# Kernel tuning notes

Hardware: AMD Instinct MI355X
Metric: run time of the kernel (lower is better)

## Reference

```python
import jax, jax.numpy as jnp
import numpy as np

B, N, C, E, K = 2, 1024, 128, 64, 20

def setup_inputs() -> dict:
    key = jax.random.key(0)
    ks = jax.random.split(key, 4)
    x = jax.random.normal(ks[0], (B, N, C), dtype=jnp.float32)
    Wl = jax.random.normal(ks[1], (C, E), dtype=jnp.float32) * 0.05
    Wr = jax.random.normal(ks[2], (C, E), dtype=jnp.float32) * 0.05
    att = jax.random.normal(ks[3], (1, E), dtype=jnp.float32) * 0.1
    bl = jnp.zeros((E,), dtype=jnp.float32)
    br = jnp.zeros((E,), dtype=jnp.float32)
    edge_index = jnp.zeros((2, 1), dtype=jnp.int64)
    batch = jnp.zeros((B * N,), dtype=jnp.int64)
    return {"x": x, "Wl": Wl, "bl": bl, "Wr": Wr, "br": br, "att": att,
            "edge_index": edge_index, "batch": batch}

def reference(x, Wl, bl, Wr, br, att, edge_index, batch):
    # x: [B, N, C]
    b, n, _ = x.shape
    x_l = x @ Wl + bl              # [B, N, E]
    x_r = x @ Wr + br              # [B, N, E]
    # dense pairwise scores: leaky_relu(x_l_i + x_r_j) . att  -> [B, N, N]
    x_cat = jax.nn.leaky_relu(x_l[:, :, None, :] + x_r[:, None, :, :], 0.2)
    alpha = jnp.einsum('bijd,d->bij', x_cat, att[0])
    alpha = jnp.nan_to_num(alpha, nan=0.0, posinf=0.0, neginf=0.0)
    k = min(K, n)
    vals, idx = jax.lax.top_k(alpha, k)            # [B, N, k]
    attention = jax.nn.softmax(vals, axis=-1).reshape(-1)  # [B*N*k]
    # edge index construction (dropout p used only in training; eval = identity)
    offset = (jnp.arange(b) * n)[:, None]                      # [B, 1]
    index_i = jnp.tile(jnp.repeat(jnp.arange(n), k)[None, :], (b, 1)) + offset
    index_j = idx.reshape(b, n * k) + offset
    new_edge_index = jnp.stack([index_i.reshape(-1), index_j.reshape(-1)], axis=0)
    return new_edge_index, attention
```

## Files before the change

### kernel.cpp

```cpp
#include <hip/hip_runtime.h>

#define Bq 2
#define Nq 1024
#define Cq 128
#define Eq 64
#define Kq 20
#define TI 8
#define THREADS 512

__global__ __launch_bounds__(128) void proj_kernel(
    const float* __restrict__ x, const float* __restrict__ Wl,
    const float* __restrict__ bl, const float* __restrict__ Wr,
    const float* __restrict__ br, const float* __restrict__ att,
    float* __restrict__ xl, float* __restrict__ xrT, float* __restrict__ rdot) {
  const int row = blockIdx.x;
  const int t = threadIdx.x;
  __shared__ float xs[Cq];
  xs[t] = x[(size_t)row * Cq + t];
  __syncthreads();
  const float* W = (t < Eq) ? Wl : Wr;
  const int e = t & 63;
  float acc = 0.f;
#pragma unroll 8
  for (int c = 0; c < Cq; ++c) acc += xs[c] * W[c * Eq + e];
  acc += (t < Eq) ? bl[e] : br[e];
  if (t < Eq) {
    xl[(size_t)row * Eq + e] = acc;
  } else {
    xrT[(size_t)e * (Bq * Nq) + row] = acc;
    float rd = acc * att[e];
#pragma unroll
    for (int m = 1; m < 64; m <<= 1) rd += __shfl_xor(rd, m);
    if (e == 0) rdot[row] = rd;
  }
}

__global__ __launch_bounds__(THREADS) void attn_kernel(
    const float* __restrict__ xl, const float* __restrict__ xrT,
    const float* __restrict__ rdot, const float* __restrict__ att,
    float* __restrict__ out) {
  const int gi0  = blockIdx.x * TI;
  const int b    = gi0 >> 10;
  const int tid  = threadIdx.x;
  const int lane = tid & 63;
  const int wave = tid >> 6;

  __shared__ float alpha[TI][Nq];
  __shared__ float xls[TI][Eq];
  __shared__ float catt[Eq];

  xls[tid >> 6][tid & 63] = xl[(size_t)gi0 * Eq + tid];
  if (tid < Eq) catt[tid] = 0.4f * att[tid];
  __syncthreads();

  {
    const int j = tid * 2;
    const float2 rd = *(const float2*)&rdot[b * Nq + j];
    float acc[TI][2];
#pragma unroll
    for (int r = 0; r < TI; ++r) { acc[r][0] = 0.6f * rd.x; acc[r][1] = 0.6f * rd.y; }
    const float* __restrict__ xrb = xrT + (size_t)b * Nq + j;
#pragma unroll
    for (int ch = 0; ch < 16; ++ch) {
      const float4 cv = *(const float4*)&catt[ch * 4];
      float4 xlv[TI];
#pragma unroll
      for (int r = 0; r < TI; ++r) xlv[r] = *(const float4*)&xls[r][ch * 4];
#pragma unroll
      for (int dd = 0; dd < 4; ++dd) {
        const float2 xv = *(const float2*)&xrb[(size_t)(ch * 4 + dd) * (Bq * Nq)];
        const float c = ((const float*)&cv)[dd];
#pragma unroll
        for (int r = 0; r < TI; ++r) {
          const float xld = ((const float*)&xlv[r])[dd];
          acc[r][0] = fmaf(fabsf(xld + xv.x), c, acc[r][0]);
          acc[r][1] = fmaf(fabsf(xld + xv.y), c, acc[r][1]);
        }
      }
    }
#pragma unroll
    for (int r = 0; r < TI; ++r)
      *(float2*)&alpha[r][j] = make_float2(acc[r][0], acc[r][1]);
  }
  __syncthreads();

  const int r = wave;
  float vals[16];
#pragma unroll
  for (int s = 0; s < 16; ++s) vals[s] = alpha[r][lane + 64 * s];
  float lv = -3.4e38f; int li = 0;
#pragma unroll
  for (int s = 0; s < 16; ++s) if (vals[s] > lv) { lv = vals[s]; li = s; }

  float m0 = 0.f, ssum = 0.f, myv = 0.f;
  int myi = 0;
  for (int round = 0; round < Kq; ++round) {
    float bv = lv;
    int   bi = (li << 6) | lane;
#pragma unroll
    for (int mm = 1; mm < 64; mm <<= 1) {
      const float ov = __shfl_xor(bv, mm);
      const int   oi = __shfl_xor(bi, mm);
      if (ov > bv || (ov == bv && oi < bi)) { bv = ov; bi = oi; }
    }
    if (round == 0) m0 = bv;
    ssum += __expf(bv - m0);
    if (lane == round) { myv = bv; myi = bi; }
    if ((bi & 63) == lane) {
#pragma unroll
      for (int s = 0; s < 16; ++s) vals[s] = (s == li) ? -3.4e38f : vals[s];
      lv = -3.4e38f; li = 0;
#pragma unroll
      for (int s = 0; s < 16; ++s) if (vals[s] > lv) { lv = vals[s]; li = s; }
    }
  }

  if (lane < Kq) {
    const int gi = gi0 + r;
    const float p = __expf(myv - m0) / ssum;
    const int base = gi * Kq + lane;
    out[base]                    = (float)gi;
    out[Bq * Nq * Kq + base]     = (float)(b * Nq + myi);
    out[2 * Bq * Nq * Kq + base] = p;
  }
}

extern "C" void kernel_launch(void* const* d_in, const int* in_sizes, int n_in,
                              void* d_out, int out_size, void* d_ws, size_t ws_size,
                              hipStream_t stream) {
  const float* x   = (const float*)d_in[0];
  const float* Wl  = (const float*)d_in[1];
  const float* bl  = (const float*)d_in[2];
  const float* Wr  = (const float*)d_in[3];
  const float* br  = (const float*)d_in[4];
  const float* att = (const float*)d_in[5];
  float* out = (float*)d_out;

  float* xl   = (float*)d_ws;
  float* xrT  = xl + (size_t)Bq * Nq * Eq;
  float* rdot = xrT + (size_t)Eq * Bq * Nq;

  proj_kernel<<<Bq * Nq, Cq, 0, stream>>>(x, Wl, bl, Wr, br, att, xl, xrT, rdot);
  attn_kernel<<<(Bq * Nq) / TI, THREADS, 0, stream>>>(xl, xrT, rdot, att, out);
}
```

Baseline: 42.53 us.

## Retile projection and score kernels, use DPP reductions for top-k selection

The projection kernel now computes four rows per block, reading x directly as float4 instead of staging it in shared memory, and reduces rdot with DPP and readlane instead of shuffles. The score kernel uses a 4x4 register tile per thread with float4 loads of xrT and rescales scores by 1/0.4, folding the 0.4 factor into the softmax exponent. The top-k argmax replaces the 6-step shuffle butterfly with DPP max and min-key reductions. This cuts shuffle latency and per-row launch overhead, but the fewer projection blocks lower parallelism and the scaling trick changes rounding slightly.

Result: faster. 41.29 us (-2.9%).

```diff
diff --git a/kernel.cpp b/kernel.cpp
--- a/kernel.cpp
+++ b/kernel.cpp
@@ -6,36 +6,75 @@
 #define Eq 64
 #define Kq 20
 #define TI 8
-#define THREADS 512
+#define BNK (Bq * Nq * Kq)
+#define NEGF (-3.0e38f)
+
+#define DPP_F(x, ctrl) __int_as_float(__builtin_amdgcn_update_dpp( \
+    __float_as_int(x), __float_as_int(x), (ctrl), 0xf, 0xf, false))
+#define DPP_I(x, ctrl) __builtin_amdgcn_update_dpp((x), (x), (ctrl), 0xf, 0xf, false)
+#define RL_F(x, l) __int_as_float(__builtin_amdgcn_readlane(__float_as_int(x), (l)))
+#define RL_I(x, l) __builtin_amdgcn_readlane((x), (l))
+#define QP_XOR1 0xB1
+#define QP_XOR2 0x4E
+#define ROR4    0x124
+#define ROR8    0x128
 
 __global__ __launch_bounds__(128) void proj_kernel(
     const float* __restrict__ x, const float* __restrict__ Wl,
     const float* __restrict__ bl, const float* __restrict__ Wr,
     const float* __restrict__ br, const float* __restrict__ att,
     float* __restrict__ xl, float* __restrict__ xrT, float* __restrict__ rdot) {
-  const int row = blockIdx.x;
+  const int r0 = blockIdx.x * 4;
   const int t = threadIdx.x;
-  __shared__ float xs[Cq];
-  xs[t] = x[(size_t)row * Cq + t];
-  __syncthreads();
-  const float* W = (t < Eq) ? Wl : Wr;
   const int e = t & 63;
-  float acc = 0.f;
+  const bool left = (t < 64);
+  const float* __restrict__ W = left ? Wl : Wr;
+  const float* __restrict__ xrow = x + (size_t)r0 * Cq;
+
+  float acc[4] = {0.f, 0.f, 0.f, 0.f};
 #pragma unroll 8
-  for (int c = 0; c < Cq; ++c) acc += xs[c] * W[c * Eq + e];
-  acc += (t < Eq) ? bl[e] : br[e];
-  if (t < Eq) {
-    xl[(size_t)row * Eq + e] = acc;
+  for (int c4 = 0; c4 < Cq / 4; ++c4) {
+    const float4 xa = *(const float4*)&xrow[c4 * 4];
+    const float4 xb = *(const float4*)&xrow[Cq + c4 * 4];
+    const float4 xc = *(const float4*)&xrow[2 * Cq + c4 * 4];
+    const float4 xd = *(const float4*)&xrow[3 * Cq + c4 * 4];
+    const float a0[4] = {xa.x, xa.y, xa.z, xa.w};
+    const float a1[4] = {xb.x, xb.y, xb.z, xb.w};
+    const float a2[4] = {xc.x, xc.y, xc.z, xc.w};
+    const float a3[4] = {xd.x, xd.y, xd.z, xd.w};
+#pragma unroll
+    for (int dd = 0; dd < 4; ++dd) {
+      const float w = W[(c4 * 4 + dd) * Eq + e];
+      acc[0] = fmaf(a0[dd], w, acc[0]);
+      acc[1] = fmaf(a1[dd], w, acc[1]);
+      acc[2] = fmaf(a2[dd], w, acc[2]);
+      acc[3] = fmaf(a3[dd], w, acc[3]);
+    }
+  }
+  const float bias = left ? bl[e] : br[e];
+#pragma unroll
+  for (int k = 0; k < 4; ++k) acc[k] += bias;
+
+  if (left) {
+#pragma unroll
+    for (int k = 0; k < 4; ++k) xl[(size_t)(r0 + k) * Eq + e] = acc[k];
   } else {
-    xrT[(size_t)e * (Bq * Nq) + row] = acc;
-    float rd = acc * att[e];
-#pragma unroll
-    for (int m = 1; m < 64; m <<= 1) rd += __shfl_xor(rd, m);
-    if (e == 0) rdot[row] = rd;
+    const float ae = att[e];
+#pragma unroll
+    for (int k = 0; k < 4; ++k) {
+      xrT[(size_t)e * (Bq * Nq) + r0 + k] = acc[k];
+      float s = acc[k] * ae;
+      s += DPP_F(s, QP_XOR1);
+      s += DPP_F(s, QP_XOR2);
+      s += DPP_F(s, ROR4);
+      s += DPP_F(s, ROR8);
+      const float sd = (RL_F(s, 0) + RL_F(s, 16)) + (RL_F(s, 32) + RL_F(s, 48));
+      if (e == 0) rdot[r0 + k] = sd;
+    }
   }
 }
 
-__global__ __launch_bounds__(THREADS) void attn_kernel(
+__global__ __launch_bounds__(512) void attn_kernel(
     const float* __restrict__ xl, const float* __restrict__ xrT,
     const float* __restrict__ rdot, const float* __restrict__ att,
     float* __restrict__ out) {
@@ -47,81 +86,103 @@
 
   __shared__ float alpha[TI][Nq];
   __shared__ float xls[TI][Eq];
-  __shared__ float catt[Eq];
 
   xls[tid >> 6][tid & 63] = xl[(size_t)gi0 * Eq + tid];
-  if (tid < Eq) catt[tid] = 0.4f * att[tid];
   __syncthreads();
 
   {
-    const int j = tid * 2;
-    const float2 rd = *(const float2*)&rdot[b * Nq + j];
-    float acc[TI][2];
-#pragma unroll
-    for (int r = 0; r < TI; ++r) { acc[r][0] = 0.6f * rd.x; acc[r][1] = 0.6f * rd.y; }
-    const float* __restrict__ xrb = xrT + (size_t)b * Nq + j;
-#pragma unroll
+    const int jt = tid & 255;
+    const int j0 = jt * 4;
+    const int rg = tid >> 8;
+    const float4 rd4 = *(const float4*)&rdot[b * Nq + j0];
+    const float rdv[4] = {rd4.x, rd4.y, rd4.z, rd4.w};
+    float acc[4][4];
+#pragma unroll
+    for (int rr = 0; rr < 4; ++rr)
+#pragma unroll
+      for (int jj = 0; jj < 4; ++jj) acc[rr][jj] = 1.5f * rdv[jj];
+
+    const float* __restrict__ xrb = xrT + (size_t)b * Nq + j0;
     for (int ch = 0; ch < 16; ++ch) {
-      const float4 cv = *(const float4*)&catt[ch * 4];
-      float4 xlv[TI];
-#pragma unroll
-      for (int r = 0; r < TI; ++r) xlv[r] = *(const float4*)&xls[r][ch * 4];
+      const float4 av4 = *(const float4*)&att[ch * 4];
+      const float av[4] = {av4.x, av4.y, av4.z, av4.w};
+      float xlr[4][4];
+#pragma unroll
+      for (int rr = 0; rr < 4; ++rr) {
+        const float4 v = *(const float4*)&xls[rg * 4 + rr][ch * 4];
+        xlr[rr][0] = v.x; xlr[rr][1] = v.y; xlr[rr][2] = v.z; xlr[rr][3] = v.w;
+      }
 #pragma unroll
       for (int dd = 0; dd < 4; ++dd) {
-        const float2 xv = *(const float2*)&xrb[(size_t)(ch * 4 + dd) * (Bq * Nq)];
-        const float c = ((const float*)&cv)[dd];
-#pragma unroll
-        for (int r = 0; r < TI; ++r) {
-          const float xld = ((const float*)&xlv[r])[dd];
-          acc[r][0] = fmaf(fabsf(xld + xv.x), c, acc[r][0]);
-          acc[r][1] = fmaf(fabsf(xld + xv.y), c, acc[r][1]);
+        const float4 xv4 = *(const float4*)&xrb[(size_t)(ch * 4 + dd) * (Bq * Nq)];
+        const float xv[4] = {xv4.x, xv4.y, xv4.z, xv4.w};
+        const float a = av[dd];
+#pragma unroll
+        for (int rr = 0; rr < 4; ++rr) {
+          const float xld = xlr[rr][dd];
+#pragma unroll
+          for (int jj = 0; jj < 4; ++jj)
+            acc[rr][jj] = fmaf(fabsf(xld + xv[jj]), a, acc[rr][jj]);
         }
       }
     }
 #pragma unroll
-    for (int r = 0; r < TI; ++r)
-      *(float2*)&alpha[r][j] = make_float2(acc[r][0], acc[r][1]);
+    for (int rr = 0; rr < 4; ++rr)
+      *(float4*)&alpha[rg * 4 + rr][j0] =
+          make_float4(acc[rr][0], acc[rr][1], acc[rr][2], acc[rr][3]);
   }
   __syncthreads();
 
-  const int r = wave;
   float vals[16];
 #pragma unroll
-  for (int s = 0; s < 16; ++s) vals[s] = alpha[r][lane + 64 * s];
-  float lv = -3.4e38f; int li = 0;
-#pragma unroll
-  for (int s = 0; s < 16; ++s) if (vals[s] > lv) { lv = vals[s]; li = s; }
+  for (int s = 0; s < 16; ++s) vals[s] = alpha[wave][lane + 64 * s];
+
+  float lv = vals[0];
+  int   pk = lane;
+#pragma unroll
+  for (int s = 1; s < 16; ++s)
+    if (vals[s] > lv) { lv = vals[s]; pk = (s << 6) | lane; }
 
   float m0 = 0.f, ssum = 0.f, myv = 0.f;
   int myi = 0;
+#pragma unroll 1
   for (int round = 0; round < Kq; ++round) {
-    float bv = lv;
-    int   bi = (li << 6) | lane;
-#pragma unroll
-    for (int mm = 1; mm < 64; mm <<= 1) {
-      const float ov = __shfl_xor(bv, mm);
-      const int   oi = __shfl_xor(bi, mm);
-      if (ov > bv || (ov == bv && oi < bi)) { bv = ov; bi = oi; }
-    }
+    float m = lv;
+    m = fmaxf(m, DPP_F(m, QP_XOR1));
+    m = fmaxf(m, DPP_F(m, QP_XOR2));
+    m = fmaxf(m, DPP_F(m, ROR4));
+    m = fmaxf(m, DPP_F(m, ROR8));
+    const float bv = fmaxf(fmaxf(RL_F(m, 0), RL_F(m, 16)),
+                           fmaxf(RL_F(m, 32), RL_F(m, 48)));
+    int key = (lv == bv) ? pk : 0x7FFFFFFF;
+    key = min(key, DPP_I(key, QP_XOR1));
+    key = min(key, DPP_I(key, QP_XOR2));
+    key = min(key, DPP_I(key, ROR4));
+    key = min(key, DPP_I(key, ROR8));
+    const int jsel = min(min(RL_I(key, 0), RL_I(key, 16)),
+                         min(RL_I(key, 32), RL_I(key, 48)));
     if (round == 0) m0 = bv;
-    ssum += __expf(bv - m0);
-    if (lane == round) { myv = bv; myi = bi; }
-    if ((bi & 63) == lane) {
-#pragma unroll
-      for (int s = 0; s < 16; ++s) vals[s] = (s == li) ? -3.4e38f : vals[s];
-      lv = -3.4e38f; li = 0;
-#pragma unroll
-      for (int s = 0; s < 16; ++s) if (vals[s] > lv) { lv = vals[s]; li = s; }
+    ssum += __expf(0.4f * (bv - m0));
+    if (lane == round) { myv = bv; myi = jsel; }
+    if (lane == (jsel & 63)) {
+      const int sk = jsel >> 6;
+#pragma unroll
+      for (int s = 0; s < 16; ++s)
+        if (s == sk) vals[s] = NEGF;
+      lv = vals[0]; pk = lane;
+#pragma unroll
+      for (int s = 1; s < 16; ++s)
+        if (vals[s] > lv) { lv = vals[s]; pk = (s << 6) | lane; }
     }
   }
 
   if (lane < Kq) {
-    const int gi = gi0 + r;
-    const float p = __expf(myv - m0) / ssum;
+    const int gi = gi0 + wave;
+    const float p = __expf(0.4f * (myv - m0)) / ssum;
     const int base = gi * Kq + lane;
-    out[base]                    = (float)gi;
-    out[Bq * Nq * Kq + base]     = (float)(b * Nq + myi);
-    out[2 * Bq * Nq * Kq + base] = p;
+    out[base]            = (float)gi;
+    out[BNK + base]      = (float)(b * Nq + myi);
+    out[2 * BNK + base]  = p;
   }
 }
 
@@ -140,6 +201,6 @@
   float* xrT  = xl + (size_t)Bq * Nq * Eq;
   float* rdot = xrT + (size_t)Eq * Bq * Nq;
 
-  proj_kernel<<<Bq * Nq, Cq, 0, stream>>>(x, Wl, bl, Wr, br, att, xl, xrT, rdot);
-  attn_kernel<<<(Bq * Nq) / TI, THREADS, 0, stream>>>(xl, xrT, rdot, att, out);
+  proj_kernel<<<(Bq * Nq) / 4, 128, 0, stream>>>(x, Wl, bl, Wr, br, att, xl, xrT, rdot);
+  attn_kernel<<<(Bq * Nq) / TI, 512, 0, stream>>>(xl, xrT, rdot, att, out);
 }
```
